# Kernel optimization log

Measured on AMD Instinct MI355X. Metric: run time of the kernel, lower is better.

Reference implementation:

```python
import jax, jax.numpy as jnp
import numpy as np

B, H, W, C = 2, 48, 48, 768
HEADS, HD = 12, 64
MLP = 3072
BOT = 384


def ln(x, w, b, eps=1e-5):
    mu = x.mean(-1, keepdims=True)
    var = ((x - mu) ** 2).mean(-1, keepdims=True)
    return (x - mu) * jax.lax.rsqrt(var + eps) * w + b


def ln_chan(x, w, b, eps=1e-6):
    # detectron2-style LayerNorm over channel dim for NCHW tensors
    mu = x.mean(1, keepdims=True)
    var = ((x - mu) ** 2).mean(1, keepdims=True)
    return (x - mu) * jax.lax.rsqrt(var + eps) * w[None, :, None, None] + b[None, :, None, None]


def conv(x, w, pad):
    return jax.lax.conv_general_dilated(x, w, (1, 1), [(pad, pad), (pad, pad)],
                                        dimension_numbers=('NCHW', 'OIHW', 'NCHW'))


def setup_inputs() -> dict:
    key = jax.random.key(0)
    ks = jax.random.split(key, 32)
    r = lambda i, shape, s=0.02: (jax.random.normal(ks[i], shape) * s).astype(jnp.float32)
    return {
        'x': jax.random.normal(ks[0], (B, H, W, C), dtype=jnp.float32),
        'norm1_w': jnp.ones((C,), jnp.float32), 'norm1_b': jnp.zeros((C,), jnp.float32),
        'qkv_w': r(1, (C, 3 * C)), 'qkv_b': r(2, (3 * C,)),
        'proj_w': r(3, (C, C)), 'proj_b': r(4, (C,)),
        'rel_pos_h': r(5, (2 * H - 1, HD)), 'rel_pos_w': r(6, (2 * W - 1, HD)),
        'norm2_w': jnp.ones((C,), jnp.float32), 'norm2_b': jnp.zeros((C,), jnp.float32),
        'fc1_w': r(7, (C, MLP)), 'fc1_b': r(8, (MLP,)),
        'fc2_w': r(9, (MLP, C)), 'fc2_b': r(10, (C,)),
        'conv1_w': r(11, (BOT, C, 1, 1)), 'rln1_w': jnp.ones((BOT,), jnp.float32), 'rln1_b': jnp.zeros((BOT,), jnp.float32),
        'conv2_w': r(12, (BOT, BOT, 3, 3)), 'rln2_w': jnp.ones((BOT,), jnp.float32), 'rln2_b': jnp.zeros((BOT,), jnp.float32),
        'conv3_w': r(13, (C, BOT, 1, 1)), 'rln3_w': r(14, (C,)), 'rln3_b': r(15, (C,)),
    }


def reference(x, norm1_w, norm1_b, qkv_w, qkv_b, proj_w, proj_b, rel_pos_h, rel_pos_w,
              norm2_w, norm2_b, fc1_w, fc1_b, fc2_w, fc2_b,
              conv1_w, rln1_w, rln1_b, conv2_w, rln2_w, rln2_b, conv3_w, rln3_w, rln3_b):
    b, h, w, c = x.shape
    hd = c // HEADS
    n = h * w
    scale = hd ** -0.5

    shortcut = x
    xn = ln(x, norm1_w, norm1_b)
    # qkv projection: (B,N,3,heads,hd) -> (3, B*heads, N, hd)
    qkv = (xn.reshape(b, n, c) @ qkv_w + qkv_b).reshape(b, n, 3, HEADS, hd)
    qkv = qkv.transpose(2, 0, 3, 1, 4).reshape(3, b * HEADS, n, hd)
    q, k, v = qkv[0], qkv[1], qkv[2]

    attn = jnp.einsum('bnd,bmd->bnm', q * scale, k)  # (B*heads, N, N)

    # decomposed relative position bias
    idx_h = jnp.arange(h)[:, None] - jnp.arange(h)[None, :] + (h - 1)
    idx_w = jnp.arange(w)[:, None] - jnp.arange(w)[None, :] + (w - 1)
    Rh = rel_pos_h[idx_h]  # (H, H, hd)
    Rw = rel_pos_w[idx_w]  # (W, W, hd)
    rq = q.reshape(b * HEADS, h, w, hd)
    rel_h = jnp.einsum('bhwc,hkc->bhwk', rq, Rh)
    rel_w = jnp.einsum('bhwc,wkc->bhwk', rq, Rw)
    attn = attn.reshape(b * HEADS, h, w, h, w) + rel_h[:, :, :, :, None] + rel_w[:, :, :, None, :]
    attn = jax.nn.softmax(attn.reshape(b * HEADS, n, n), axis=-1)

    out = (attn @ v).reshape(b, HEADS, h, w, hd).transpose(0, 2, 3, 1, 4).reshape(b, h, w, c)
    x = shortcut + (out @ proj_w + proj_b)

    # MLP
    xn = ln(x, norm2_w, norm2_b)
    hdn = jax.nn.gelu(xn @ fc1_w + fc1_b, approximate=False)
    x = x + (hdn @ fc2_w + fc2_b)

    # residual bottleneck block (NCHW)
    y = x.transpose(0, 3, 1, 2)
    o = jax.nn.gelu(ln_chan(conv(y, conv1_w, 0), rln1_w, rln1_b), approximate=False)
    o = jax.nn.gelu(ln_chan(conv(o, conv2_w, 1), rln2_w, rln2_b), approximate=False)
    o = ln_chan(conv(o, conv3_w, 0), rln3_w, rln3_b)
    y = y + o
    return y.transpose(0, 2, 3, 1)
```

## Files before the change

### kernel.cpp

```cpp
#include <hip/hip_runtime.h>

typedef unsigned short ushort_t;
typedef __attribute__((ext_vector_type(8))) short bf16x8;
typedef __attribute__((ext_vector_type(4))) float f32x4;

#define DEV static __device__ __forceinline__

DEV ushort_t f2bf(float f){
  union { float f; unsigned u; } v; v.f = f;
  unsigned r = v.u + 0x7FFFu + ((v.u >> 16) & 1u);
  return (ushort_t)(r >> 16);
}
DEV float bf2f(ushort_t h){
  union { unsigned u; float f; } v; v.u = ((unsigned)h) << 16;
  return v.f;
}
DEV float gelu_f(float x){ return 0.5f * x * (1.f + erff(x * 0.70710678118654752f)); }

#define MFMA16(a,b,c) __builtin_amdgcn_mfma_f32_16x16x32_bf16((a),(b),(c),0,0,0)

DEV void gld16(const ushort_t* g, ushort_t* l){
  __builtin_amdgcn_global_load_lds(
      (const __attribute__((address_space(1))) unsigned int*)g,
      (__attribute__((address_space(3))) unsigned int*)l, 16, 0, 0);
}


__global__ __launch_bounds__(256) void transpose_cast_kernel(
    const float* __restrict__ src, ushort_t* __restrict__ dst, int K, int N){
  __shared__ float tile[32][33];
  int k0 = blockIdx.x * 32, n0 = blockIdx.y * 32;
  int tx = threadIdx.x & 31, ty = threadIdx.x >> 5;
  #pragma unroll
  for(int i = ty; i < 32; i += 8) tile[i][tx] = src[(long)(k0+i)*N + n0 + tx];
  __syncthreads();
  #pragma unroll
  for(int i = ty; i < 32; i += 8) dst[(long)(n0+i)*K + k0 + tx] = f2bf(tile[tx][i]);
}

__global__ void cast_kernel(const float* __restrict__ src, ushort_t* __restrict__ dst, int n){
  int i = blockIdx.x*256 + threadIdx.x;
  if(i < n) dst[i] = f2bf(src[i]);
}

__global__ void conv2_reorder_kernel(const float* __restrict__ src, ushort_t* __restrict__ dst){
  int i = blockIdx.x*256 + threadIdx.x;
  if(i >= 384*3456) return;
  int co = i / 3456, r = i - co*3456;
  int dy = r / 1152; int r2 = r - dy*1152;
  int dx = r2 / 384; int ci = r2 - dx*384;
  dst[i] = f2bf(src[((co*384 + ci)*3 + dy)*3 + dx]);
}

__global__ __launch_bounds__(256) void vt_kernel(
    const ushort_t* __restrict__ v, ushort_t* __restrict__ vt){
  __shared__ __align__(16) ushort_t t[64][72];
  int bh = blockIdx.y, nt = blockIdx.x;
  int tid = threadIdx.x;
  #pragma unroll
  for(int p=0;p<2;p++){
    int item = tid + p*256;
    int tok = item >> 3, ch = item & 7;
    bf16x8 vv = *(const bf16x8*)(v + ((long)(bh*2304 + nt*64 + tok))*64 + ch*8);
    #pragma unroll
    for(int j=0;j<8;j++) t[ch*8+j][tok] = (ushort_t)vv[j];
  }
  __syncthreads();
  #pragma unroll
  for(int p=0;p<2;p++){
    int item = tid + p*256;
    int d = item >> 3, c2 = item & 7;
    bf16x8 rd = *(const bf16x8*)&t[d][c2*8];
    *(bf16x8*)(vt + ((long)(bh*64 + d))*2304 + nt*64 + c2*8) = rd;
  }
}

template<int D, bool GELU, bool RES, bool PADOUT>
__global__ __launch_bounds__(256) void ln_kernel(
    const float* __restrict__ in, const float* __restrict__ w, const float* __restrict__ bv,
    const float* __restrict__ res, float eps,
    ushort_t* __restrict__ outb, float* __restrict__ outf){
  constexpr int PER = D/64;
  int lane = threadIdx.x & 63, wid = threadIdx.x >> 6;
  long row = (long)blockIdx.x*4 + wid;
  const float* ip = in + row*D;
  float x[PER]; float s = 0.f;
  #pragma unroll
  for(int i=0;i<PER;i++){ x[i] = ip[i*64 + lane]; s += x[i]; }
  #pragma unroll
  for(int o=32;o>=1;o>>=1) s += __shfl_xor(s, o);
  float mu = s * (1.f/D);
  float vs = 0.f;
  #pragma unroll
  for(int i=0;i<PER;i++){ float d = x[i]-mu; vs += d*d; }
  #pragma unroll
  for(int o=32;o>=1;o>>=1) vs += __shfl_xor(vs, o);
  float rstd = rsqrtf(vs*(1.f/D) + eps);
  long obase;
  if constexpr(PADOUT){
    int bb = (int)(row / 2304); int rm = (int)(row - (long)bb*2304);
    int y = rm / 48, xx = rm - y*48;
    obase = ((long)((bb*50 + y+1)*50) + (xx+1))*384;
  } else obase = row*D;
  #pragma unroll
  for(int i=0;i<PER;i++){
    int c = i*64 + lane;
    float y = (x[i]-mu)*rstd*w[c] + bv[c];
    if constexpr(GELU) y = gelu_f(y);
    if constexpr(RES)  y += res[row*D + c];
    if(outb) outb[obase + c] = f2bf(y);
    if(outf) outf[row*D + c] = y;
  }
}

__global__ __launch_bounds__(256) void relpos_mfma_kernel(
    const ushort_t* __restrict__ q, const ushort_t* __restrict__ tabh,
    const ushort_t* __restrict__ tabw,
    float* __restrict__ relh, float* __restrict__ relw){
  const int bh = blockIdx.y;
  const bool isH = (blockIdx.z == 0);
  const int w = threadIdx.x >> 6, lane = threadIdx.x & 63;
  const int la = lane & 15, grp = lane >> 4;
  const int pos0 = blockIdx.x*4 + w;
  const ushort_t* tab = isH ? tabh : tabw;
  float* outp = isH ? relh : relw;
  const ushort_t* qbase = q + (long)bh*2304*64;

  bf16x8 bf0[3], bf1[3];
  #pragma unroll
  for(int ni=0;ni<3;ni++){
    int dpos = pos0 - (ni*16+la) + 47;
    const ushort_t* tp = tab + dpos*64 + grp*8;
    bf0[ni] = *(const bf16x8*)tp;
    bf1[ni] = *(const bf16x8*)(tp+32);
  }
  #pragma unroll
  for(int mi=0;mi<3;mi++){
    int arow = mi*16 + la;
    long na = isH ? ((long)pos0*48 + arow) : ((long)arow*48 + pos0);
    const ushort_t* qp = qbase + na*64 + grp*8;
    bf16x8 a0 = *(const bf16x8*)qp;
    bf16x8 a1 = *(const bf16x8*)(qp+32);
    f32x4 c[3];
    #pragma unroll
    for(int ni=0;ni<3;ni++){
      f32x4 z; z[0]=0.f; z[1]=0.f; z[2]=0.f; z[3]=0.f;
      z = MFMA16(a0, bf0[ni], z);
      z = MFMA16(a1, bf1[ni], z);
      c[ni] = z;
    }
    #pragma unroll
    for(int ni=0;ni<3;ni++)
      #pragma unroll
      for(int r=0;r<4;r++){
        int orow = mi*16 + grp*4 + r;
        long no = isH ? ((long)pos0*48 + orow) : ((long)orow*48 + pos0);
        outp[((long)bh*2304 + no)*48 + ni*16 + la] = c[ni][r] * 8.0f;
      }
  }
}

template<int BM, int EPI, bool IM2COL>
__global__ __launch_bounds__(256) void gemm_kernel(
    const ushort_t* __restrict__ A, const ushort_t* __restrict__ Wt,
    const float* __restrict__ bias, const float* __restrict__ res,
    float* __restrict__ outf, ushort_t* __restrict__ ob0,
    ushort_t* __restrict__ ob1, ushort_t* __restrict__ ob2,
    int N, int Kdim){
  constexpr int FR = BM/32;
  __shared__ __align__(16) ushort_t Asm[BM*64];
  __shared__ __align__(16) ushort_t Bsm[BM*64];
  const int tid = threadIdx.x, lane = tid & 63, w = tid >> 6;
  const int wm = w >> 1, wn = w & 1;
  const int la = lane & 15, grp = lane >> 4;
  const int m0 = blockIdx.y * BM, n0 = blockIdx.x * BM;
  f32x4 acc[FR][FR];
  #pragma unroll
  for(int i=0;i<FR;i++)
    #pragma unroll
    for(int j=0;j<FR;j++)
      #pragma unroll
      for(int r=0;r<4;r++) acc[i][j][r] = 0.f;

  const int srw = lane >> 3;
  const int scs = ((lane&7) ^ srw) * 8;
  for(int k0 = 0; k0 < Kdim; k0 += 64){
    if(k0) __syncthreads();
    #pragma unroll
    for(int t=0;t<FR;t++){
      int r = w*(BM/4) + t*8 + srw;
      const ushort_t* ga;
      if constexpr(IM2COL){
        int m = m0 + r;
        int bb = m / 2304; int rm = m - bb*2304;
        int y = rm / 48, x = rm - y*48;
        int dy = k0 / 1152; int r2 = k0 - dy*1152;
        int dx = r2 / 384;  int cb = r2 - dx*384;
        ga = A + (((long)((bb*50 + y+dy)*50) + (x+dx))*384 + cb + scs);
      } else {
        ga = A + (long)(m0+r)*Kdim + k0 + scs;
      }
      gld16(ga, &Asm[(w*(BM/4)+t*8)*64]);
      gld16(Wt + (long)(n0+r)*Kdim + k0 + scs, &Bsm[(w*(BM/4)+t*8)*64]);
    }
    __syncthreads();
    #pragma unroll
    for(int ks=0; ks<2; ks++){
      bf16x8 af[FR], bfm[FR];
      #pragma unroll
      for(int mi=0;mi<FR;mi++){
        int row = wm*(BM/2) + mi*16 + la;
        af[mi] = *(const bf16x8*)&Asm[row*64 + ((((ks<<2)+grp) ^ (row&7))*8)];
      }
      #pragma unroll
      for(int ni=0;ni<FR;ni++){
        int row = wn*(BM/2) + ni*16 + la;
        bfm[ni] = *(const bf16x8*)&Bsm[row*64 + ((((ks<<2)+grp) ^ (row&7))*8)];
      }
      #pragma unroll
      for(int mi=0;mi<FR;mi++)
        #pragma unroll
        for(int ni=0;ni<FR;ni++)
          acc[mi][ni] = MFMA16(af[mi], bfm[ni], acc[mi][ni]);
    }
  }
  #pragma unroll
  for(int mi=0;mi<FR;mi++)
  #pragma unroll
  for(int ni=0;ni<FR;ni++)
  #pragma unroll
  for(int r=0;r<4;r++){
    int mm = m0 + wm*(BM/2) + mi*16 + grp*4 + r;
    int nn = n0 + wn*(BM/2) + ni*16 + la;
    float v = acc[mi][ni][r];
    if constexpr(EPI == 0){
      outf[(long)mm*N + nn] = v;
    } else if constexpr(EPI == 1){
      v += bias[nn];
      int s = nn / 768; int rem = nn - s*768;
      int head = rem >> 6, d = rem & 63;
      if(s == 0) v *= 0.125f;
      int bb = mm / 2304; int nloc = mm - bb*2304;
      long idx = ((long)((bb*12+head)*2304 + nloc))*64 + d;
      ushort_t hv = f2bf(v);
      if(s == 0) ob0[idx] = hv; else if(s == 1) ob1[idx] = hv; else ob2[idx] = hv;
    } else if constexpr(EPI == 2){
      v += bias[nn] + res[(long)mm*N + nn];
      outf[(long)mm*N + nn] = v;
    } else if constexpr(EPI == 3){
      v = gelu_f(v + bias[nn]);
      ob0[(long)mm*N + nn] = f2bf(v);
    } else if constexpr(EPI == 4){
      v += bias[nn] + res[(long)mm*N + nn];
      outf[(long)mm*N + nn] = v;
      ob0[(long)mm*N + nn] = f2bf(v);
    }
  }
}

#define NSPLIT 3
#define NTS 12
__global__ __launch_bounds__(256) void attn_kernel(
    const ushort_t* __restrict__ Q, const ushort_t* __restrict__ Kb,
    const ushort_t* __restrict__ VT, const float* __restrict__ relh,
    const float* __restrict__ relw, float* __restrict__ Opart,
    float* __restrict__ mpart, float* __restrict__ lpart){
  __shared__ __align__(16) ushort_t Kl[2][64*64];
  __shared__ __align__(16) ushort_t Vl[2][64*64];
  const int bh = blockIdx.y, qt = blockIdx.x, sp = blockIdx.z;
  const int tid = threadIdx.x, lane = tid & 63, w = tid >> 6;
  const int la = lane & 15, grp = lane >> 4;
  const int qg = qt*64 + w*16 + la;
  const long row = (long)bh*2304 + qg;

  const ushort_t* qp = Q + row*64 + grp*8;
  const bf16x8 qa0 = *(const bf16x8*)qp;
  const bf16x8 qa1 = *(const bf16x8*)(qp + 32);

  const ushort_t* kg = Kb + (long)bh*2304*64 + (long)sp*NTS*64*64;
  const ushort_t* vg = VT + (long)bh*64*2304;

  f32x4 rh4[4], rw4[3];
  {
    const float* rhq = relh + row*48 + sp*16;
    #pragma unroll
    for(int i=0;i<4;i++) rh4[i] = *(const f32x4*)(rhq + 4*i);
    const float* rwq = relw + row*48 + grp*4;
    #pragma unroll
    for(int c=0;c<3;c++) rw4[c] = *(const f32x4*)(rwq + 16*c);
  }

  const int srw = lane >> 3;
  const int scs = ((lane&7) ^ srw) * 8;

  f32x4 acc[4];
  #pragma unroll
  for(int nf=0;nf<4;nf++){ acc[nf][0]=0.f; acc[nf][1]=0.f; acc[nf][2]=0.f; acc[nf][3]=0.f; }
  float m_run = -3e38f, l_run = 0.f;

  #pragma unroll
  for(int t=0;t<2;t++){
    int r = w*16 + t*8 + srw;
    gld16(kg + (long)r*64 + scs, &Kl[0][(w*16+t*8)*64]);
    gld16(vg + (long)r*2304 + sp*NTS*64 + scs, &Vl[0][(w*16+t*8)*64]);
  }

  #pragma unroll
  for(int j=0;j<NTS;j++){
    const int cur = j & 1;
    asm volatile("s_waitcnt vmcnt(0)" ::: "memory");
    __builtin_amdgcn_sched_barrier(0);
    __builtin_amdgcn_s_barrier();
    __builtin_amdgcn_sched_barrier(0);
    if(j+1 < NTS){
      #pragma unroll
      for(int t=0;t<2;t++){
        int r = w*16 + t*8 + srw;
        gld16(kg + ((long)((j+1)*64 + r))*64 + scs, &Kl[cur^1][(w*16+t*8)*64]);
        gld16(vg + (long)r*2304 + (sp*NTS+j+1)*64 + scs, &Vl[cur^1][(w*16+t*8)*64]);
      }
    }
    f32x4 s[4];
    __builtin_amdgcn_s_setprio(1);
    #pragma unroll
    for(int nf=0;nf<4;nf++){
      const ushort_t* kl = &Kl[cur][(nf*16+la)*64];
      bf16x8 k0 = *(const bf16x8*)(kl + ((grp ^ (la&7))*8));
      bf16x8 k1 = *(const bf16x8*)(kl + (((4+grp) ^ (la&7))*8));
      f32x4 z; z[0]=0.f; z[1]=0.f; z[2]=0.f; z[3]=0.f;
      z = MFMA16(k0, qa0, z);
      z = MFMA16(k1, qa1, z);
      s[nf] = z;
    }
    __builtin_amdgcn_s_setprio(0);
    const int h0 = (4*j)/3;
    const float rha = rh4[h0>>2][h0&3];
    const float rhb = rh4[(h0+1)>>2][(h0+1)&3];
    float vals[16]; float lmax = -3e38f;
    #pragma unroll
    for(int nf=0;nf<4;nf++){
      const int cp = (j%3) + nf;
      const float rh = (cp >= 3) ? rhb : rha;
      const int c = (cp >= 3) ? cp-3 : cp;
      #pragma unroll
      for(int r=0;r<4;r++){
        float sv = s[nf][r] + rh + rw4[c][r];
        vals[nf*4+r] = sv;
        lmax = fmaxf(lmax, sv);
      }
    }
    lmax = fmaxf(lmax, __shfl_xor(lmax,16));
    lmax = fmaxf(lmax, __shfl_xor(lmax,32));
    const float mnew = fmaxf(m_run, lmax);
    const float alpha = __expf(m_run - mnew);
    m_run = mnew;
    float p[16]; float psum = 0.f;
    #pragma unroll
    for(int i=0;i<16;i++){ p[i] = __expf(vals[i]-mnew); psum += p[i]; }
    psum += __shfl_xor(psum,16);
    psum += __shfl_xor(psum,32);
    l_run = l_run*alpha + psum;
    unsigned pk[4][2];
    #pragma unroll
    for(int nf=0;nf<4;nf++)
      #pragma unroll
      for(int h=0;h<2;h++)
        pk[nf][h] = (unsigned)f2bf(p[nf*4+2*h]) | ((unsigned)f2bf(p[nf*4+2*h+1]) << 16);
    #pragma unroll
    for(int nf=0;nf<4;nf++)
      #pragma unroll
      for(int r=0;r<4;r++) acc[nf][r] *= alpha;
    #pragma unroll
    for(int ks=0; ks<2; ks++){
      unsigned wd[4];
      #pragma unroll
      for(int j2=0;j2<4;j2++){
        int src = la + 16*(((grp&1)<<1) + (j2>>1));
        unsigned wA = __shfl(pk[2*ks  ][j2&1], src);
        unsigned wB = __shfl(pk[2*ks+1][j2&1], src);
        wd[j2] = (grp >= 2) ? wB : wA;
      }
      union { unsigned u[4]; bf16x8 v; } pa;
      pa.u[0]=wd[0]; pa.u[1]=wd[1]; pa.u[2]=wd[2]; pa.u[3]=wd[3];
      __builtin_amdgcn_s_setprio(1);
      #pragma unroll
      for(int nf=0;nf<4;nf++){
        const ushort_t* vl = &Vl[cur][(nf*16+la)*64];
        bf16x8 vb = *(const bf16x8*)(vl + ((((ks<<2)+grp) ^ (la&7))*8));
        acc[nf] = MFMA16(vb, pa.v, acc[nf]);
      }
      __builtin_amdgcn_s_setprio(0);
    }
  }
  float* op = Opart + ((long)sp*55296 + row)*64;
  #pragma unroll
  for(int nf=0;nf<4;nf++)
    *(f32x4*)(op + nf*16 + grp*4) = acc[nf];
  if(grp == 0){
    mpart[(long)sp*55296 + row] = m_run;
    lpart[(long)sp*55296 + row] = l_run;
  }
}

__global__ __launch_bounds__(256) void attn_merge_kernel(
    const float* __restrict__ Opart, const float* __restrict__ mpart,
    const float* __restrict__ lpart, ushort_t* __restrict__ outp){
  int wid = threadIdx.x >> 6, lane = threadIdx.x & 63;
  long row = (long)blockIdx.x*4 + wid;
  int bh = (int)(row / 2304); int n = (int)(row - (long)bh*2304);
  int b = bh / 12, head = bh - b*12;
  float m0 = mpart[row], m1 = mpart[55296+row], m2 = mpart[2*55296+row];
  float ms = fmaxf(m0, fmaxf(m1, m2));
  float w0 = __expf(m0-ms), w1 = __expf(m1-ms), w2 = __expf(m2-ms);
  float l = w0*lpart[row] + w1*lpart[55296+row] + w2*lpart[2*55296+row];
  float o = w0*Opart[row*64+lane] + w1*Opart[(55296+row)*64+lane] + w2*Opart[(2*55296+row)*64+lane];
  outp[((long)b*2304+n)*768 + head*64 + lane] = f2bf(o / l);
}

extern "C" void kernel_launch(void* const* d_in, const int* in_sizes, int n_in,
                              void* d_out, int out_size, void* d_ws, size_t ws_size,
                              hipStream_t stream){
  const float* x     = (const float*)d_in[0];
  const float* n1w   = (const float*)d_in[1];
  const float* n1b   = (const float*)d_in[2];
  const float* qkvw  = (const float*)d_in[3];
  const float* qkvb  = (const float*)d_in[4];
  const float* projw = (const float*)d_in[5];
  const float* projb = (const float*)d_in[6];
  const float* rph   = (const float*)d_in[7];
  const float* rpw   = (const float*)d_in[8];
  const float* n2w   = (const float*)d_in[9];
  const float* n2b   = (const float*)d_in[10];
  const float* fc1w  = (const float*)d_in[11];
  const float* fc1b  = (const float*)d_in[12];
  const float* fc2w  = (const float*)d_in[13];
  const float* fc2b  = (const float*)d_in[14];
  const float* c1w   = (const float*)d_in[15];
  const float* r1w   = (const float*)d_in[16];
  const float* r1b   = (const float*)d_in[17];
  const float* c2w   = (const float*)d_in[18];
  const float* r2w   = (const float*)d_in[19];
  const float* r2b   = (const float*)d_in[20];
  const float* c3w   = (const float*)d_in[21];
  const float* r3w   = (const float*)d_in[22];
  const float* r3b   = (const float*)d_in[23];
  float* out = (float*)d_out;

  char* base = (char*)d_ws;
  size_t off = 0;
  auto carve = [&](size_t bytes)->char*{
    char* p = base + off;
    off += (bytes + 255) & ~(size_t)255;
    return p;
  };
  const long T = 4608;

  ushort_t* wqkvT = (ushort_t*)carve((size_t)2304*768*2);
  ushort_t* wprojT= (ushort_t*)carve((size_t)768*768*2);
  ushort_t* wfc1T = (ushort_t*)carve((size_t)3072*768*2);
  ushort_t* wfc2T = (ushort_t*)carve((size_t)768*3072*2);
  ushort_t* wc1   = (ushort_t*)carve((size_t)384*768*2);
  ushort_t* wc2   = (ushort_t*)carve((size_t)384*3456*2);
  ushort_t* wc3   = (ushort_t*)carve((size_t)768*384*2);
  ushort_t* tabhb = (ushort_t*)carve((size_t)95*64*2);
  ushort_t* tabwb = (ushort_t*)carve((size_t)95*64*2);
  ushort_t* xn1   = (ushort_t*)carve((size_t)T*768*2);
  ushort_t* qb    = (ushort_t*)carve((size_t)24*2304*64*2);
  ushort_t* kbuf  = (ushort_t*)carve((size_t)24*2304*64*2);
  ushort_t* vbuf  = (ushort_t*)carve((size_t)24*2304*64*2);
  ushort_t* vbufT = (ushort_t*)carve((size_t)24*2304*64*2);
  float*    relh  = (float*)carve((size_t)24*2304*48*4);
  float*    relw  = (float*)carve((size_t)24*2304*48*4);
  float*    Opart = (float*)carve((size_t)3*55296*64*4);
  float*    mpart = (float*)carve((size_t)3*55296*4);
  float*    lpart = (float*)carve((size_t)3*55296*4);
  ushort_t* attno = (ushort_t*)carve((size_t)T*768*2);
  float*    x1    = (float*)carve((size_t)T*768*4);
  ushort_t* xn2   = (ushort_t*)carve((size_t)T*768*2);
  ushort_t* hmlp  = (ushort_t*)carve((size_t)T*3072*2);
  float*    x2    = (float*)carve((size_t)T*768*4);
  ushort_t* x2b   = (ushort_t*)carve((size_t)T*768*2);
  float*    c1    = (float*)carve((size_t)T*384*4);
  ushort_t* o1pad = (ushort_t*)carve((size_t)2*50*50*384*2);
  float*    c2    = (float*)carve((size_t)T*384*4);
  ushort_t* o2    = (ushort_t*)carve((size_t)T*384*2);
  float*    c3    = (float*)carve((size_t)T*768*4);
  (void)ws_size; (void)in_sizes; (void)n_in; (void)out_size;

  transpose_cast_kernel<<<dim3(24,72),256,0,stream>>>(qkvw, wqkvT, 768, 2304);
  transpose_cast_kernel<<<dim3(24,24),256,0,stream>>>(projw, wprojT, 768, 768);
  transpose_cast_kernel<<<dim3(24,96),256,0,stream>>>(fc1w, wfc1T, 768, 3072);
  transpose_cast_kernel<<<dim3(96,24),256,0,stream>>>(fc2w, wfc2T, 3072, 768);
  cast_kernel<<<dim3(1152),256,0,stream>>>(c1w, wc1, 384*768);
  conv2_reorder_kernel<<<dim3(5184),256,0,stream>>>(c2w, wc2);
  cast_kernel<<<dim3(1152),256,0,stream>>>(c3w, wc3, 768*384);
  cast_kernel<<<dim3(24),256,0,stream>>>(rph, tabhb, 95*64);
  cast_kernel<<<dim3(24),256,0,stream>>>(rpw, tabwb, 95*64);
  hipMemsetAsync(o1pad, 0, (size_t)2*50*50*384*2, stream);

  ln_kernel<768,false,false,false><<<dim3(1152),256,0,stream>>>(x, n1w, n1b, nullptr, 1e-5f, xn1, nullptr);
  gemm_kernel<128,1,false><<<dim3(18,36),256,0,stream>>>(xn1, wqkvT, qkvb, nullptr, nullptr, qb, kbuf, vbuf, 2304, 768);
  vt_kernel<<<dim3(36,24),256,0,stream>>>(vbuf, vbufT);
  relpos_mfma_kernel<<<dim3(12,24,2),256,0,stream>>>(qb, tabhb, tabwb, relh, relw);
  attn_kernel<<<dim3(36,24,3),256,0,stream>>>(qb, kbuf, vbufT, relh, relw, Opart, mpart, lpart);
  attn_merge_kernel<<<dim3(13824),256,0,stream>>>(Opart, mpart, lpart, attno);
  gemm_kernel<64,2,false><<<dim3(12,72),256,0,stream>>>(attno, wprojT, projb, x, x1, nullptr, nullptr, nullptr, 768, 768);
  ln_kernel<768,false,false,false><<<dim3(1152),256,0,stream>>>(x1, n2w, n2b, nullptr, 1e-5f, xn2, nullptr);
  gemm_kernel<128,3,false><<<dim3(24,36),256,0,stream>>>(xn2, wfc1T, fc1b, nullptr, nullptr, hmlp, nullptr, nullptr, 3072, 768);
  gemm_kernel<64,4,false><<<dim3(12,72),256,0,stream>>>(hmlp, wfc2T, fc2b, x1, x2, x2b, nullptr, nullptr, 768, 3072);
  gemm_kernel<64,0,false><<<dim3(6,72),256,0,stream>>>(x2b, wc1, nullptr, nullptr, c1, nullptr, nullptr, nullptr, 384, 768);
  ln_kernel<384,true,false,true><<<dim3(1152),256,0,stream>>>(c1, r1w, r1b, nullptr, 1e-6f, o1pad, nullptr);
  gemm_kernel<64,0,true><<<dim3(6,72),256,0,stream>>>(o1pad, wc2, nullptr, nullptr, c2, nullptr, nullptr, nullptr, 384, 3456);
  ln_kernel<384,true,false,false><<<dim3(1152),256,0,stream>>>(c2, r2w, r2b, nullptr, 1e-6f, o2, nullptr);
  gemm_kernel<64,0,false><<<dim3(12,72),256,0,stream>>>(o2, wc3, nullptr, nullptr, c3, nullptr, nullptr, nullptr, 768, 384);
  ln_kernel<768,false,true,false><<<dim3(1152),256,0,stream>>>(c3, r3w, r3b, x2, 1e-6f, nullptr, out);
}
```

Measured before the change: 509.9 us.

## Merge weight prep launches and widen attention blocks to 128 queries with 2-way split

Folds the four weight transpose launches and the five cast/reorder launches into two combined kernels, cutting launch overhead. The attention kernel now runs 512 threads covering 128 query rows, so each K/V tile staged in shared memory is reused by twice as many queries. The key-split count drops from 3 to 2, which halves the number of partial results the merge kernel reads. It also uses a packed bf16 convert instruction and reads the relative-position height bias directly from global memory inside the loop. The trade-off is fewer blocks in the grid (864 instead of 2592) and longer serial loops per block, which may reduce occupancy and latency hiding.

```diff
diff --git a/kernel.cpp b/kernel.cpp
--- a/kernel.cpp
+++ b/kernel.cpp
@@ -26,10 +26,19 @@
 }
 
 
-__global__ __launch_bounds__(256) void transpose_cast_kernel(
-    const float* __restrict__ src, ushort_t* __restrict__ dst, int K, int N){
+__global__ __launch_bounds__(256) void transpose_all_kernel(
+    const float* __restrict__ s0, const float* __restrict__ s1,
+    const float* __restrict__ s2, const float* __restrict__ s3,
+    ushort_t* __restrict__ d0, ushort_t* __restrict__ d1,
+    ushort_t* __restrict__ d2, ushort_t* __restrict__ d3){
   __shared__ float tile[32][33];
-  int k0 = blockIdx.x * 32, n0 = blockIdx.y * 32;
+  int b = blockIdx.x;
+  const float* src; ushort_t* dst; int K, N, bx, by;
+  if(b < 1728){ src=s0; dst=d0; K=768;  N=2304; bx=b%24;          by=b/24; }
+  else if(b < 2304){ int c=b-1728; src=s1; dst=d1; K=768;  N=768;  bx=c%24; by=c/24; }
+  else if(b < 4608){ int c=b-2304; src=s2; dst=d2; K=768;  N=3072; bx=c%24; by=c/24; }
+  else             { int c=b-4608; src=s3; dst=d3; K=3072; N=768;  bx=c%96; by=c/96; }
+  int k0 = bx*32, n0 = by*32;
   int tx = threadIdx.x & 31, ty = threadIdx.x >> 5;
   #pragma unroll
   for(int i = ty; i < 32; i += 8) tile[i][tx] = src[(long)(k0+i)*N + n0 + tx];
@@ -38,18 +47,25 @@
   for(int i = ty; i < 32; i += 8) dst[(long)(n0+i)*K + k0 + tx] = f2bf(tile[tx][i]);
 }
 
-__global__ void cast_kernel(const float* __restrict__ src, ushort_t* __restrict__ dst, int n){
+__global__ void cast_all_kernel(
+    const float* __restrict__ c1w, const float* __restrict__ c2w,
+    const float* __restrict__ c3w, const float* __restrict__ rph,
+    const float* __restrict__ rpw,
+    ushort_t* __restrict__ wc1, ushort_t* __restrict__ wc2,
+    ushort_t* __restrict__ wc3, ushort_t* __restrict__ tabh,
+    ushort_t* __restrict__ tabw){
   int i = blockIdx.x*256 + threadIdx.x;
-  if(i < n) dst[i] = f2bf(src[i]);
-}
-
-__global__ void conv2_reorder_kernel(const float* __restrict__ src, ushort_t* __restrict__ dst){
-  int i = blockIdx.x*256 + threadIdx.x;
-  if(i >= 384*3456) return;
-  int co = i / 3456, r = i - co*3456;
-  int dy = r / 1152; int r2 = r - dy*1152;
-  int dx = r2 / 384; int ci = r2 - dx*384;
-  dst[i] = f2bf(src[((co*384 + ci)*3 + dy)*3 + dx]);
+  if(i < 294912){ wc1[i] = f2bf(c1w[i]); }
+  else if(i < 1622016){
+    int j = i - 294912;
+    int co = j / 3456, r = j - co*3456;
+    int dy = r / 1152; int r2 = r - dy*1152;
+    int dx = r2 / 384; int ci = r2 - dx*384;
+    wc2[j] = f2bf(c2w[((co*384 + ci)*3 + dy)*3 + dx]);
+  }
+  else if(i < 1916928){ int j = i - 1622016; wc3[j] = f2bf(c3w[j]); }
+  else if(i < 1923008){ int j = i - 1916928; tabh[j] = f2bf(rph[j]); }
+  else if(i < 1929088){ int j = i - 1923008; tabw[j] = f2bf(rpw[j]); }
 }
 
 __global__ __launch_bounds__(256) void vt_kernel(
@@ -258,9 +274,9 @@
   }
 }
 
-#define NSPLIT 3
-#define NTS 12
-__global__ __launch_bounds__(256) void attn_kernel(
+#define NSPLIT 2
+#define NTS 18
+__global__ __launch_bounds__(512) void attn_kernel(
     const ushort_t* __restrict__ Q, const ushort_t* __restrict__ Kb,
     const ushort_t* __restrict__ VT, const float* __restrict__ relh,
     const float* __restrict__ relw, float* __restrict__ Opart,
@@ -270,21 +286,20 @@
   const int bh = blockIdx.y, qt = blockIdx.x, sp = blockIdx.z;
   const int tid = threadIdx.x, lane = tid & 63, w = tid >> 6;
   const int la = lane & 15, grp = lane >> 4;
-  const int qg = qt*64 + w*16 + la;
+  const int qg = qt*128 + w*16 + la;
   const long row = (long)bh*2304 + qg;
+  const int key0 = sp*NTS*64;
 
   const ushort_t* qp = Q + row*64 + grp*8;
   const bf16x8 qa0 = *(const bf16x8*)qp;
   const bf16x8 qa1 = *(const bf16x8*)(qp + 32);
 
-  const ushort_t* kg = Kb + (long)bh*2304*64 + (long)sp*NTS*64*64;
-  const ushort_t* vg = VT + (long)bh*64*2304;
-
-  f32x4 rh4[4], rw4[3];
+  const ushort_t* kg = Kb + ((long)bh*2304 + key0)*64;
+  const ushort_t* vg = VT + (long)bh*64*2304 + key0;
+  const float* rhq = relh + row*48;
+
+  f32x4 rw4[3];
   {
-    const float* rhq = relh + row*48 + sp*16;
-    #pragma unroll
-    for(int i=0;i<4;i++) rh4[i] = *(const f32x4*)(rhq + 4*i);
     const float* rwq = relw + row*48 + grp*4;
     #pragma unroll
     for(int c=0;c<3;c++) rw4[c] = *(const f32x4*)(rwq + 16*c);
@@ -292,106 +307,112 @@
 
   const int srw = lane >> 3;
   const int scs = ((lane&7) ^ srw) * 8;
+  const int strow = w*8 + srw;
 
   f32x4 acc[4];
   #pragma unroll
   for(int nf=0;nf<4;nf++){ acc[nf][0]=0.f; acc[nf][1]=0.f; acc[nf][2]=0.f; acc[nf][3]=0.f; }
   float m_run = -3e38f, l_run = 0.f;
 
-  #pragma unroll
-  for(int t=0;t<2;t++){
-    int r = w*16 + t*8 + srw;
-    gld16(kg + (long)r*64 + scs, &Kl[0][(w*16+t*8)*64]);
-    gld16(vg + (long)r*2304 + sp*NTS*64 + scs, &Vl[0][(w*16+t*8)*64]);
-  }
-
-  #pragma unroll
-  for(int j=0;j<NTS;j++){
-    const int cur = j & 1;
-    asm volatile("s_waitcnt vmcnt(0)" ::: "memory");
-    __builtin_amdgcn_sched_barrier(0);
-    __builtin_amdgcn_s_barrier();
-    __builtin_amdgcn_sched_barrier(0);
-    if(j+1 < NTS){
-      #pragma unroll
-      for(int t=0;t<2;t++){
-        int r = w*16 + t*8 + srw;
-        gld16(kg + ((long)((j+1)*64 + r))*64 + scs, &Kl[cur^1][(w*16+t*8)*64]);
-        gld16(vg + (long)r*2304 + (sp*NTS+j+1)*64 + scs, &Vl[cur^1][(w*16+t*8)*64]);
-      }
+  gld16(kg + (long)strow*64 + scs, &Kl[0][(w*8)*64]);
+  gld16(vg + (long)strow*2304 + scs, &Vl[0][(w*8)*64]);
+
+  for(int t=0; t<6; t++){
+    #define ATTN_ITER(u)                                                         \
+    {                                                                            \
+      const int j = 3*t + (u);                                                   \
+      const int cur = (t + (u)) & 1;                                             \
+      asm volatile("s_waitcnt vmcnt(0)" ::: "memory");                           \
+      __builtin_amdgcn_sched_barrier(0);                                         \
+      __builtin_amdgcn_s_barrier();                                              \
+      __builtin_amdgcn_sched_barrier(0);                                         \
+      const int h0 = sp*24 + 4*t + (u);                                          \
+      const float rha = rhq[h0];                                                 \
+      const float rhb = rhq[h0+1];                                               \
+      if(j+1 < NTS){                                                             \
+        gld16(kg + ((long)((j+1)*64 + strow))*64 + scs, &Kl[cur^1][(w*8)*64]);   \
+        gld16(vg + (long)strow*2304 + (j+1)*64 + scs, &Vl[cur^1][(w*8)*64]);     \
+      }                                                                          \
+      f32x4 s[4];                                                                \
+      __builtin_amdgcn_s_setprio(1);                                             \
+      _Pragma("unroll")                                                          \
+      for(int nf=0;nf<4;nf++){                                                   \
+        const ushort_t* kl = &Kl[cur][(nf*16+la)*64];                            \
+        bf16x8 k0 = *(const bf16x8*)(kl + ((grp ^ (la&7))*8));                   \
+        bf16x8 k1 = *(const bf16x8*)(kl + (((4+grp) ^ (la&7))*8));               \
+        f32x4 z; z[0]=0.f; z[1]=0.f; z[2]=0.f; z[3]=0.f;                         \
+        z = MFMA16(k0, qa0, z);                                                  \
+        z = MFMA16(k1, qa1, z);                                                  \
+        s[nf] = z;                                                               \
+      }                                                                          \
+      __builtin_amdgcn_s_setprio(0);                                             \
+      float lmax = -3e38f;                                                       \
+      _Pragma("unroll")                                                          \
+      for(int nf=0;nf<4;nf++){                                                   \
+        const int cp = (u) + nf;                                                 \
+        const float rh = (cp >= 3) ? rhb : rha;                                  \
+        const int c = (cp >= 3) ? cp-3 : cp;                                     \
+        _Pragma("unroll")                                                        \
+        for(int r=0;r<4;r++){                                                    \
+          s[nf][r] += rh + rw4[c][r];                                            \
+          lmax = fmaxf(lmax, s[nf][r]);                                          \
+        }                                                                        \
+      }                                                                          \
+      lmax = fmaxf(lmax, __shfl_xor(lmax,16));                                   \
+      lmax = fmaxf(lmax, __shfl_xor(lmax,32));                                   \
+      const float mnew = fmaxf(m_run, lmax);                                     \
+      const float alpha = __expf(m_run - mnew);                                  \
+      m_run = mnew;                                                              \
+      float psum = 0.f;                                                          \
+      _Pragma("unroll")                                                          \
+      for(int nf=0;nf<4;nf++)                                                    \
+        _Pragma("unroll")                                                        \
+        for(int r=0;r<4;r++){                                                    \
+          s[nf][r] = __expf(s[nf][r] - mnew);                                    \
+          psum += s[nf][r];                                                      \
+        }                                                                        \
+      psum += __shfl_xor(psum,16);                                               \
+      psum += __shfl_xor(psum,32);                                               \
+      l_run = l_run*alpha + psum;                                                \
+      unsigned pk[4][2];                                                         \
+      _Pragma("unroll")                                                          \
+      for(int nf=0;nf<4;nf++)                                                    \
+        _Pragma("unroll")                                                        \
+        for(int h=0;h<2;h++)                                                     \
+          asm("v_cvt_pk_bf16_f32 %0, %1, %2"                                     \
+              : "=v"(pk[nf][h]) : "v"(s[nf][2*h]), "v"(s[nf][2*h+1]));           \
+      _Pragma("unroll")                                                          \
+      for(int nf=0;nf<4;nf++)                                                    \
+        _Pragma("unroll")                                                        \
+        for(int r=0;r<4;r++) acc[nf][r] *= alpha;                                \
+      _Pragma("unroll")                                                          \
+      for(int ks=0; ks<2; ks++){                                                 \
+        unsigned wd[4];                                                          \
+        _Pragma("unroll")                                                        \
+        for(int j2=0;j2<4;j2++){                                                 \
+          int src = la + 16*(((grp&1)<<1) + (j2>>1));                            \
+          unsigned wA = __shfl(pk[2*ks  ][j2&1], src);                           \
+          unsigned wB = __shfl(pk[2*ks+1][j2&1], src);                           \
+          wd[j2] = (grp >= 2) ? wB : wA;                                         \
+        }                                                                        \
+        union { unsigned uu[4]; bf16x8 v; } pa;                                  \
+        pa.uu[0]=wd[0]; pa.uu[1]=wd[1]; pa.uu[2]=wd[2]; pa.uu[3]=wd[3];          \
+        __builtin_amdgcn_s_setprio(1);                                           \
+        _Pragma("unroll")                                                        \
+        for(int nf=0;nf<4;nf++){                                                 \
+          const ushort_t* vl = &Vl[cur][(nf*16+la)*64];                          \
+          bf16x8 vb = *(const bf16x8*)(vl + ((((ks<<2)+grp) ^ (la&7))*8));       \
+          acc[nf] = MFMA16(vb, pa.v, acc[nf]);                                   \
+        }                                                                        \
+        __builtin_amdgcn_s_setprio(0);                                           \
+      }                                                                          \
     }
-    f32x4 s[4];
-    __builtin_amdgcn_s_setprio(1);
-    #pragma unroll
-    for(int nf=0;nf<4;nf++){
-      const ushort_t* kl = &Kl[cur][(nf*16+la)*64];
-      bf16x8 k0 = *(const bf16x8*)(kl + ((grp ^ (la&7))*8));
-      bf16x8 k1 = *(const bf16x8*)(kl + (((4+grp) ^ (la&7))*8));
-      f32x4 z; z[0]=0.f; z[1]=0.f; z[2]=0.f; z[3]=0.f;
-      z = MFMA16(k0, qa0, z);
-      z = MFMA16(k1, qa1, z);
-      s[nf] = z;
-    }
-    __builtin_amdgcn_s_setprio(0);
-    const int h0 = (4*j)/3;
-    const float rha = rh4[h0>>2][h0&3];
-    const float rhb = rh4[(h0+1)>>2][(h0+1)&3];
-    float vals[16]; float lmax = -3e38f;
-    #pragma unroll
-    for(int nf=0;nf<4;nf++){
-      const int cp = (j%3) + nf;
-      const float rh = (cp >= 3) ? rhb : rha;
-      const int c = (cp >= 3) ? cp-3 : cp;
-      #pragma unroll
-      for(int r=0;r<4;r++){
-        float sv = s[nf][r] + rh + rw4[c][r];
-        vals[nf*4+r] = sv;
-        lmax = fmaxf(lmax, sv);
-      }
-    }
-    lmax = fmaxf(lmax, __shfl_xor(lmax,16));
-    lmax = fmaxf(lmax, __shfl_xor(lmax,32));
-    const float mnew = fmaxf(m_run, lmax);
-    const float alpha = __expf(m_run - mnew);
-    m_run = mnew;
-    float p[16]; float psum = 0.f;
-    #pragma unroll
-    for(int i=0;i<16;i++){ p[i] = __expf(vals[i]-mnew); psum += p[i]; }
-    psum += __shfl_xor(psum,16);
-    psum += __shfl_xor(psum,32);
-    l_run = l_run*alpha + psum;
-    unsigned pk[4][2];
-    #pragma unroll
-    for(int nf=0;nf<4;nf++)
-      #pragma unroll
-      for(int h=0;h<2;h++)
-        pk[nf][h] = (unsigned)f2bf(p[nf*4+2*h]) | ((unsigned)f2bf(p[nf*4+2*h+1]) << 16);
-    #pragma unroll
-    for(int nf=0;nf<4;nf++)
-      #pragma unroll
-      for(int r=0;r<4;r++) acc[nf][r] *= alpha;
-    #pragma unroll
-    for(int ks=0; ks<2; ks++){
-      unsigned wd[4];
-      #pragma unroll
-      for(int j2=0;j2<4;j2++){
-        int src = la + 16*(((grp&1)<<1) + (j2>>1));
-        unsigned wA = __shfl(pk[2*ks  ][j2&1], src);
-        unsigned wB = __shfl(pk[2*ks+1][j2&1], src);
-        wd[j2] = (grp >= 2) ? wB : wA;
-      }
-      union { unsigned u[4]; bf16x8 v; } pa;
-      pa.u[0]=wd[0]; pa.u[1]=wd[1]; pa.u[2]=wd[2]; pa.u[3]=wd[3];
-      __builtin_amdgcn_s_setprio(1);
-      #pragma unroll
-      for(int nf=0;nf<4;nf++){
-        const ushort_t* vl = &Vl[cur][(nf*16+la)*64];
-        bf16x8 vb = *(const bf16x8*)(vl + ((((ks<<2)+grp) ^ (la&7))*8));
-        acc[nf] = MFMA16(vb, pa.v, acc[nf]);
-      }
-      __builtin_amdgcn_s_setprio(0);
-    }
-  }
+    ATTN_ITER(0)
+    ATTN_ITER(1)
+    ATTN_ITER(2)
+    #undef ATTN_ITER
+  }
+
   float* op = Opart + ((long)sp*55296 + row)*64;
   #pragma unroll
   for(int nf=0;nf<4;nf++)
@@ -409,11 +430,11 @@
   long row = (long)blockIdx.x*4 + wid;
   int bh = (int)(row / 2304); int n = (int)(row - (long)bh*2304);
   int b = bh / 12, head = bh - b*12;
-  float m0 = mpart[row], m1 = mpart[55296+row], m2 = mpart[2*55296+row];
-  float ms = fmaxf(m0, fmaxf(m1, m2));
-  float w0 = __expf(m0-ms), w1 = __expf(m1-ms), w2 = __expf(m2-ms);
-  float l = w0*lpart[row] + w1*lpart[55296+row] + w2*lpart[2*55296+row];
-  float o = w0*Opart[row*64+lane] + w1*Opart[(55296+row)*64+lane] + w2*Opart[(2*55296+row)*64+lane];
+  float m0 = mpart[row], m1 = mpart[55296+row];
+  float ms = fmaxf(m0, m1);
+  float w0 = __expf(m0-ms), w1 = __expf(m1-ms);
+  float l = w0*lpart[row] + w1*lpart[55296+row];
+  float o = w0*Opart[row*64+lane] + w1*Opart[(55296+row)*64+lane];
   outp[((long)b*2304+n)*768 + head*64 + lane] = f2bf(o / l);
 }
 
@@ -471,9 +492,9 @@
   ushort_t* vbufT = (ushort_t*)carve((size_t)24*2304*64*2);
   float*    relh  = (float*)carve((size_t)24*2304*48*4);
   float*    relw  = (float*)carve((size_t)24*2304*48*4);
-  float*    Opart = (float*)carve((size_t)3*55296*64*4);
-  float*    mpart = (float*)carve((size_t)3*55296*4);
-  float*    lpart = (float*)carve((size_t)3*55296*4);
+  float*    Opart = (float*)carve((size_t)2*55296*64*4);
+  float*    mpart = (float*)carve((size_t)2*55296*4);
+  float*    lpart = (float*)carve((size_t)2*55296*4);
   ushort_t* attno = (ushort_t*)carve((size_t)T*768*2);
   float*    x1    = (float*)carve((size_t)T*768*4);
   ushort_t* xn2   = (ushort_t*)carve((size_t)T*768*2);
@@ -487,22 +508,17 @@
   float*    c3    = (float*)carve((size_t)T*768*4);
   (void)ws_size; (void)in_sizes; (void)n_in; (void)out_size;
 
-  transpose_cast_kernel<<<dim3(24,72),256,0,stream>>>(qkvw, wqkvT, 768, 2304);
-  transpose_cast_kernel<<<dim3(24,24),256,0,stream>>>(projw, wprojT, 768, 768);
-  transpose_cast_kernel<<<dim3(24,96),256,0,stream>>>(fc1w, wfc1T, 768, 3072);
-  transpose_cast_kernel<<<dim3(96,24),256,0,stream>>>(fc2w, wfc2T, 3072, 768);
-  cast_kernel<<<dim3(1152),256,0,stream>>>(c1w, wc1, 384*768);
-  conv2_reorder_kernel<<<dim3(5184),256,0,stream>>>(c2w, wc2);
-  cast_kernel<<<dim3(1152),256,0,stream>>>(c3w, wc3, 768*384);
-  cast_kernel<<<dim3(24),256,0,stream>>>(rph, tabhb, 95*64);
-  cast_kernel<<<dim3(24),256,0,stream>>>(rpw, tabwb, 95*64);
+  transpose_all_kernel<<<dim3(6912),256,0,stream>>>(qkvw, projw, fc1w, fc2w,
+                                                    wqkvT, wprojT, wfc1T, wfc2T);
+  cast_all_kernel<<<dim3(7536),256,0,stream>>>(c1w, c2w, c3w, rph, rpw,
+                                               wc1, wc2, wc3, tabhb, tabwb);
   hipMemsetAsync(o1pad, 0, (size_t)2*50*50*384*2, stream);
 
   ln_kernel<768,false,false,false><<<dim3(1152),256,0,stream>>>(x, n1w, n1b, nullptr, 1e-5f, xn1, nullptr);
   gemm_kernel<128,1,false><<<dim3(18,36),256,0,stream>>>(xn1, wqkvT, qkvb, nullptr, nullptr, qb, kbuf, vbuf, 2304, 768);
   vt_kernel<<<dim3(36,24),256,0,stream>>>(vbuf, vbufT);
   relpos_mfma_kernel<<<dim3(12,24,2),256,0,stream>>>(qb, tabhb, tabwb, relh, relw);
-  attn_kernel<<<dim3(36,24,3),256,0,stream>>>(qb, kbuf, vbufT, relh, relw, Opart, mpart, lpart);
+  attn_kernel<<<dim3(18,24,2),512,0,stream>>>(qb, kbuf, vbufT, relh, relw, Opart, mpart, lpart);
   attn_merge_kernel<<<dim3(13824),256,0,stream>>>(Opart, mpart, lpart, attno);
   gemm_kernel<64,2,false><<<dim3(12,72),256,0,stream>>>(attno, wprojT, projb, x, x1, nullptr, nullptr, nullptr, 768, 768);
   ln_kernel<768,false,false,false><<<dim3(1152),256,0,stream>>>(x1, n2w, n2b, nullptr, 1e-5f, xn2, nullptr);
```

Measured after the change: 436.8 us. -14.3%, faster.
